# Performance work log

Measured on AMD Instinct MI355X. Metric: run time of the kernel, lower is better.

## Reference

```python
import jax, jax.numpy as jnp
import numpy as np

N, T, IN, E, H, OUT = 4096, 256, 2, 64, 128, 2


def setup_inputs() -> dict:
    key = jax.random.key(0)
    ks = jax.random.split(key, 10)
    s = 0.05
    return {
        "x": jax.random.normal(ks[0], (N, T, IN), dtype=jnp.float32),
        "W_in": jax.random.normal(ks[1], (E, IN), dtype=jnp.float32) * s,
        "b_in": jax.random.normal(ks[2], (E,), dtype=jnp.float32) * s,
        "W_ih": jax.random.normal(ks[3], (4 * H, E), dtype=jnp.float32) * s,
        "W_hh": jax.random.normal(ks[4], (4 * H, H), dtype=jnp.float32) * s,
        "b_ih": jax.random.normal(ks[5], (4 * H,), dtype=jnp.float32) * s,
        "b_hh": jax.random.normal(ks[6], (4 * H,), dtype=jnp.float32) * s,
        "W_out": jax.random.normal(ks[7], (OUT, H), dtype=jnp.float32) * s,
        "b_out": jax.random.normal(ks[8], (OUT,), dtype=jnp.float32) * s,
    }


def reference(x, W_in, b_in, W_ih, W_hh, b_ih, b_hh, W_out, b_out):
    # x: [N, T, IN]. burn_in_steps = -1 (teacher forcing every step), use_mask=False,
    # rel_out=True, rtype='lstm'. PyTorch LSTMCell gate order: i, f, g, o.
    n = x.shape[0]
    h0 = jnp.zeros((n, H), dtype=x.dtype)
    c0 = jnp.zeros((n, H), dtype=x.dtype)

    def step(carry, x_t):
        h, c = carry
        embed = jax.nn.relu(x_t @ W_in.T + b_in)              # [N, E]
        gates = embed @ W_ih.T + b_ih + h @ W_hh.T + b_hh     # [N, 4H]
        i, f, g, o = jnp.split(gates, 4, axis=-1)
        i = jax.nn.sigmoid(i)
        f = jax.nn.sigmoid(f)
        g = jnp.tanh(g)
        o = jax.nn.sigmoid(o)
        c_new = f * c + i * g
        h_new = o * jnp.tanh(c_new)
        y_t = h_new @ W_out.T + b_out + x_t                   # rel_out: residual add
        return (h_new, c_new), y_t

    xs = jnp.swapaxes(x, 0, 1)                                 # [T, N, IN]
    _, ys = jax.lax.scan(step, (h0, c0), xs)                   # ys: [T, N, OUT]
    return jnp.swapaxes(ys, 0, 1)                              # [N, T, OUT]
```

## Files before the change

### kernel.cpp

```cpp
#include <hip/hip_runtime.h>


#define T_LEN 256
#define ROWS  16
#define NT    4
#define KT    6
#define ASTR  200

typedef __attribute__((ext_vector_type(8))) short short8;
typedef __attribute__((ext_vector_type(4))) float f32x4;
typedef __attribute__((ext_vector_type(2))) float f32x2;

__device__ __forceinline__ unsigned short f2bf(float f) {
  unsigned u = __builtin_bit_cast(unsigned, f);
  u += 0x7fffu + ((u >> 16) & 1u);
  return (unsigned short)(u >> 16);
}
__device__ __forceinline__ f32x2 exp2v(f32x2 x) {
  return (f32x2){__builtin_amdgcn_exp2f(x[0]), __builtin_amdgcn_exp2f(x[1])};
}
__device__ __forceinline__ f32x2 rcpv(f32x2 x) {
  return (f32x2){__builtin_amdgcn_rcpf(x[0]), __builtin_amdgcn_rcpf(x[1])};
}

__device__ __forceinline__ f32x2 ewpair(f32x2 i, f32x2 f, f32x2 g, f32x2 o, f32x2& c) {
  const float K1 = -1.4426950408889634f, K2 = -2.8853900817779268f;
  f32x2 ei = exp2v(i * K1);
  f32x2 ef = exp2v(f * K1);
  f32x2 eg = exp2v(g * K2);
  f32x2 eo = exp2v(o * K1);
  f32x2 t1 = ei + 1.f, tf = ef + 1.f, t2 = eg + 1.f, t3 = 1.f - eg, to = eo + 1.f;
  f32x2 q1 = t1 * t2;
  f32x2 num = c * q1 + t3 * tf;
  f32x2 cn = num * rcpv(q1 * tf);
  c = cn;
  f32x2 cc = __builtin_elementwise_min(
      __builtin_elementwise_max(cn, (f32x2){-20.f, -20.f}), (f32x2){20.f, 20.f});
  f32x2 ec = exp2v(cc * K2);
  return (1.f - ec) * rcpv(to * (ec + 1.f));
}

__global__ __launch_bounds__(512, 2) void lstm_persist(
    const float* __restrict__ x,    const float* __restrict__ W_in,
    const float* __restrict__ b_in, const float* __restrict__ W_ih,
    const float* __restrict__ W_hh, const float* __restrict__ b_ih,
    const float* __restrict__ b_hh, const float* __restrict__ W_out,
    const float* __restrict__ b_out, float* __restrict__ out)
{
  __shared__ __align__(16) float xsT[2 * T_LEN][ROWS];
  __shared__ __align__(16) unsigned short Abuf[3][ROWS][ASTR];
  __shared__ float WinS[128];
  __shared__ float binS[64];

  const int tid  = threadIdx.x;
  const int w    = tid >> 6;
  const int l    = tid & 63;
  const int l15  = l & 15;
  const int lq   = l >> 4;
  const int u    = w * 16 + l15;
  const int row0 = lq * 4;

  const float* xg = x + (size_t)blockIdx.x * ROWS * 2 * T_LEN;
  for (int i = tid; i < ROWS * 2 * T_LEN / 4; i += 512) {
    float4 v = ((const float4*)xg)[i];
    int fi = i * 4, r = fi >> 9, c0 = fi & 511;
    xsT[c0][r] = v.x; xsT[c0 + 1][r] = v.y; xsT[c0 + 2][r] = v.z; xsT[c0 + 3][r] = v.w;
  }
  if (tid < 128) WinS[tid] = W_in[tid];
  if (tid < 64)  binS[tid] = b_in[tid];

  short8 fb[NT][KT];
  f32x4  biasv[NT];
  #pragma unroll
  for (int t = 0; t < NT; ++t) {
    const int grow = t * 128 + u;
    const float bv = b_ih[grow] + b_hh[grow];
    biasv[t] = (f32x4){bv, bv, bv, bv};
    #pragma unroll
    for (int kt = 0; kt < KT; ++kt) {
      const int kk = kt * 32 + lq * 8;
      const float* src = (kk < 64) ? (W_ih + grow * 64 + kk)
                                   : (W_hh + grow * 128 + (kk - 64));
      float4 lo = *(const float4*)src;
      float4 hi = *(const float4*)(src + 4);
      short8 f;
      f[0] = (short)f2bf(lo.x); f[1] = (short)f2bf(lo.y);
      f[2] = (short)f2bf(lo.z); f[3] = (short)f2bf(lo.w);
      f[4] = (short)f2bf(hi.x); f[5] = (short)f2bf(hi.y);
      f[6] = (short)f2bf(hi.z); f[7] = (short)f2bf(hi.w);
      fb[t][kt] = f;
    }
  }
  short8 fbY[4];
  #pragma unroll
  for (int kt = 0; kt < 4; ++kt) {
    short8 fy = {0, 0, 0, 0, 0, 0, 0, 0};
    if (l15 < 2) {
      const float* src = W_out + l15 * 128 + kt * 32 + lq * 8;
      #pragma unroll
      for (int j = 0; j < 8; ++j) fy[j] = (short)f2bf(src[j]);
    }
    fbY[kt] = fy;
  }
  const float bout_r = (l15 < 2) ? b_out[l15] : 0.f;

  __syncthreads();

  auto embed_to = [&](unsigned short (*buf)[ASTR], int t) {
    const int r = tid >> 5;
    const float x0 = xsT[2 * t][r], x1 = xsT[2 * t + 1][r];
    #pragma unroll
    for (int s = 0; s < 2; ++s) {
      const int e = (tid & 31) + s * 32;
      float v = fmaf(x1, WinS[2 * e + 1], fmaf(x0, WinS[2 * e], binS[e]));
      buf[r][e] = f2bf(v > 0.f ? v : 0.f);
    }
  };

  for (int i = tid; i < ROWS * 128; i += 512)
    Abuf[0][i >> 7][64 + (i & 127)] = 0;
  embed_to(Abuf[0], 0);
  embed_to(Abuf[1], 1);
  __syncthreads();

  f32x4 accA[NT], accB[NT];
  {
    const short8 a0 = *(const short8*)&Abuf[0][l15][lq * 8];
    const short8 a1 = *(const short8*)&Abuf[0][l15][32 + lq * 8];
    #pragma unroll
    for (int n = 0; n < NT; ++n) {
      f32x4 acc = biasv[n];
      acc = __builtin_amdgcn_mfma_f32_16x16x32_bf16(a0, fb[n][0], acc, 0, 0, 0);
      acc = __builtin_amdgcn_mfma_f32_16x16x32_bf16(a1, fb[n][1], acc, 0, 0, 0);
      accA[n] = acc;
    }
  }

  f32x2 c01 = {0.f, 0.f}, c23 = {0.f, 0.f};
  const size_t obase = (size_t)blockIdx.x * ROWS * 2 * T_LEN;

  auto step = [&](int t, unsigned short (*bR)[ASTR], unsigned short (*bW)[ASTR],
                  unsigned short (*bE)[ASTR], f32x4 (&accC)[NT], f32x4 (&accN)[NT]) {
    short8 ah[4];
    #pragma unroll
    for (int kt = 0; kt < 4; ++kt)
      ah[kt] = *(const short8*)&bR[l15][(kt + 2) * 32 + lq * 8];
    #pragma unroll
    for (int kt = 0; kt < 4; ++kt) {
      #pragma unroll
      for (int n = 0; n < NT; ++n)
        accC[n] = __builtin_amdgcn_mfma_f32_16x16x32_bf16(ah[kt], fb[n][kt + 2], accC[n], 0, 0, 0);
    }

    f32x4 accY;
    if (w == 0) {
      const int tt = (t > 0) ? t - 1 : 0;
      #pragma unroll
      for (int q = 0; q < 4; ++q)
        accY[q] = (l15 < 2) ? (bout_r + xsT[2 * tt + l15][row0 + q]) : 0.f;
      #pragma unroll
      for (int kt = 0; kt < 4; ++kt)
        accY = __builtin_amdgcn_mfma_f32_16x16x32_bf16(ah[kt], fbY[kt], accY, 0, 0, 0);
    }

    if (t + 1 < T_LEN) {
      const short8 a0 = *(const short8*)&bW[l15][lq * 8];
      const short8 a1 = *(const short8*)&bW[l15][32 + lq * 8];
      #pragma unroll
      for (int n = 0; n < NT; ++n) {
        f32x4 acc = biasv[n];
        acc = __builtin_amdgcn_mfma_f32_16x16x32_bf16(a0, fb[n][0], acc, 0, 0, 0);
        acc = __builtin_amdgcn_mfma_f32_16x16x32_bf16(a1, fb[n][1], acc, 0, 0, 0);
        accN[n] = acc;
      }
    }

    {
      f32x2 i01 = {accC[0][0], accC[0][1]}, f01 = {accC[1][0], accC[1][1]};
      f32x2 g01 = {accC[2][0], accC[2][1]}, o01 = {accC[3][0], accC[3][1]};
      f32x2 h01 = ewpair(i01, f01, g01, o01, c01);
      bW[row0 + 0][64 + u] = f2bf(h01[0]);
      bW[row0 + 1][64 + u] = f2bf(h01[1]);
      f32x2 i23 = {accC[0][2], accC[0][3]}, f23 = {accC[1][2], accC[1][3]};
      f32x2 g23 = {accC[2][2], accC[2][3]}, o23 = {accC[3][2], accC[3][3]};
      f32x2 h23 = ewpair(i23, f23, g23, o23, c23);
      bW[row0 + 2][64 + u] = f2bf(h23[0]);
      bW[row0 + 3][64 + u] = f2bf(h23[1]);
    }

    if (t + 2 < T_LEN) embed_to(bE, t + 2);

    if (w == 0 && t > 0 && l15 < 2) {
      #pragma unroll
      for (int q = 0; q < 4; ++q)
        out[obase + (size_t)(row0 + q) * (2 * T_LEN) + 2 * (t - 1) + l15] = accY[q];
    }

    __syncthreads();
  };

  unsigned short (*B0)[ASTR] = Abuf[0];
  unsigned short (*B1)[ASTR] = Abuf[1];
  unsigned short (*B2)[ASTR] = Abuf[2];

  for (int t = 0; t < 252; t += 6) {
    step(t + 0, B0, B1, B2, accA, accB);
    step(t + 1, B1, B2, B0, accB, accA);
    step(t + 2, B2, B0, B1, accA, accB);
    step(t + 3, B0, B1, B2, accB, accA);
    step(t + 4, B1, B2, B0, accA, accB);
    step(t + 5, B2, B0, B1, accB, accA);
  }
  step(252, B0, B1, B2, accA, accB);
  step(253, B1, B2, B0, accB, accA);
  step(254, B2, B0, B1, accA, accB);
  step(255, B0, B1, B2, accB, accA);

  if (w == 0) {
    short8 ah[4];
    #pragma unroll
    for (int kt = 0; kt < 4; ++kt)
      ah[kt] = *(const short8*)&Abuf[1][l15][(kt + 2) * 32 + lq * 8];
    f32x4 accY;
    #pragma unroll
    for (int q = 0; q < 4; ++q)
      accY[q] = (l15 < 2) ? (bout_r + xsT[2 * 255 + l15][row0 + q]) : 0.f;
    #pragma unroll
    for (int kt = 0; kt < 4; ++kt)
      accY = __builtin_amdgcn_mfma_f32_16x16x32_bf16(ah[kt], fbY[kt], accY, 0, 0, 0);
    if (l15 < 2) {
      #pragma unroll
      for (int q = 0; q < 4; ++q)
        out[obase + (size_t)(row0 + q) * (2 * T_LEN) + 2 * 255 + l15] = accY[q];
    }
  }
}

extern "C" void kernel_launch(void* const* d_in, const int* in_sizes, int n_in,
                              void* d_out, int out_size, void* d_ws, size_t ws_size,
                              hipStream_t stream) {
  const float* x     = (const float*)d_in[0];
  const float* W_in  = (const float*)d_in[1];
  const float* b_in  = (const float*)d_in[2];
  const float* W_ih  = (const float*)d_in[3];
  const float* W_hh  = (const float*)d_in[4];
  const float* b_ih  = (const float*)d_in[5];
  const float* b_hh  = (const float*)d_in[6];
  const float* W_out = (const float*)d_in[7];
  const float* b_out = (const float*)d_in[8];
  float* out = (float*)d_out;

  lstm_persist<<<dim3(256), dim3(512), 0, stream>>>(
      x, W_in, b_in, W_ih, W_hh, b_ih, b_hh, W_out, b_out, out);
}
```

Before: 262.8 us.

## Split LSTM gate K-reduction across two wave halves with LDS partial exchange

Doubles the block to 1024 threads and splits the per-step recurrent MFMA reduction along K between two 8-wave halves. Partial gate sums are exchanged through a new LDS buffer, and each half then runs the elementwise cell update for two of the four rows. The A buffer also switches to an XOR-swizzled layout to cut bank conflicts. The aim is to halve the serial MFMA chain per wave on the critical recurrent path, at the cost of an extra __syncthreads per step and extra LDS traffic.

Result: slower. 494.2 us (+88.0%).

```diff
diff --git a/kernel.cpp b/kernel.cpp
--- a/kernel.cpp
+++ b/kernel.cpp
@@ -2,10 +2,7 @@
 
 
 #define T_LEN 256
-#define ROWS  16
-#define NT    4
-#define KT    6
-#define ASTR  200
+#define NROW  16
 
 typedef __attribute__((ext_vector_type(8))) short short8;
 typedef __attribute__((ext_vector_type(4))) float f32x4;
@@ -40,28 +37,31 @@
   return (1.f - ec) * rcpv(to * (ec + 1.f));
 }
 
-__global__ __launch_bounds__(512, 2) void lstm_persist(
+__global__ __launch_bounds__(1024, 4) void lstm_persist(
     const float* __restrict__ x,    const float* __restrict__ W_in,
     const float* __restrict__ b_in, const float* __restrict__ W_ih,
     const float* __restrict__ W_hh, const float* __restrict__ b_ih,
     const float* __restrict__ b_hh, const float* __restrict__ W_out,
     const float* __restrict__ b_out, float* __restrict__ out)
 {
-  __shared__ __align__(16) float xsT[2 * T_LEN][ROWS];
-  __shared__ __align__(16) unsigned short Abuf[3][ROWS][ASTR];
+  __shared__ __align__(16) float xsT[2 * T_LEN][NROW];
+  __shared__ __align__(16) unsigned short Abuf[3][NROW * 192];
+  __shared__ __align__(16) float Xbuf[2][8][64 * 12];
+  __shared__ __align__(16) float Ybuf[64 * 4];
   __shared__ float WinS[128];
   __shared__ float binS[64];
 
-  const int tid  = threadIdx.x;
-  const int w    = tid >> 6;
-  const int l    = tid & 63;
-  const int l15  = l & 15;
-  const int lq   = l >> 4;
-  const int u    = w * 16 + l15;
-  const int row0 = lq * 4;
-
-  const float* xg = x + (size_t)blockIdx.x * ROWS * 2 * T_LEN;
-  for (int i = tid; i < ROWS * 2 * T_LEN / 4; i += 512) {
+  const int tid = threadIdx.x;
+  const int w   = tid >> 6;
+  const int l   = tid & 63;
+  const int l15 = l & 15;
+  const int lq  = l >> 4;
+  const int kh  = w >> 3;
+  const int w8  = w & 7;
+  const int u   = w8 * 16 + l15;
+
+  const float* xg = x + (size_t)blockIdx.x * NROW * 2 * T_LEN;
+  for (int i = tid; i < NROW * 2 * T_LEN / 4; i += 1024) {
     float4 v = ((const float4*)xg)[i];
     int fi = i * 4, r = fi >> 9, c0 = fi & 511;
     xsT[c0][r] = v.x; xsT[c0 + 1][r] = v.y; xsT[c0 + 2][r] = v.z; xsT[c0 + 3][r] = v.w;
@@ -69,16 +69,20 @@
   if (tid < 128) WinS[tid] = W_in[tid];
   if (tid < 64)  binS[tid] = b_in[tid];
 
-  short8 fb[NT][KT];
-  f32x4  biasv[NT];
+  const int kt0 = kh ? 1 : 0;
+  const int ktA = kh ? 4 : 2;
+  const int ktB = kh ? 5 : 3;
+
+  short8 fb[4][3];
+  float  bias4[4];
   #pragma unroll
-  for (int t = 0; t < NT; ++t) {
-    const int grow = t * 128 + u;
-    const float bv = b_ih[grow] + b_hh[grow];
-    biasv[t] = (f32x4){bv, bv, bv, bv};
-    #pragma unroll
-    for (int kt = 0; kt < KT; ++kt) {
-      const int kk = kt * 32 + lq * 8;
+  for (int g = 0; g < 4; ++g) {
+    const int grow = g * 128 + u;
+    bias4[g] = (kh == 0) ? (b_ih[grow] + b_hh[grow]) : 0.f;
+    const int kts[3] = {kt0, ktA, ktB};
+    #pragma unroll
+    for (int j = 0; j < 3; ++j) {
+      const int kk = kts[j] * 32 + lq * 8;
       const float* src = (kk < 64) ? (W_ih + grow * 64 + kk)
                                    : (W_hh + grow * 128 + (kk - 64));
       float4 lo = *(const float4*)src;
@@ -88,151 +92,165 @@
       f[2] = (short)f2bf(lo.z); f[3] = (short)f2bf(lo.w);
       f[4] = (short)f2bf(hi.x); f[5] = (short)f2bf(hi.y);
       f[6] = (short)f2bf(hi.z); f[7] = (short)f2bf(hi.w);
-      fb[t][kt] = f;
-    }
-  }
-  short8 fbY[4];
+      fb[g][j] = f;
+    }
+  }
+  short8 fbY[2];
   #pragma unroll
-  for (int kt = 0; kt < 4; ++kt) {
+  for (int j = 0; j < 2; ++j) {
     short8 fy = {0, 0, 0, 0, 0, 0, 0, 0};
+    const int kt = ktA + j;
     if (l15 < 2) {
-      const float* src = W_out + l15 * 128 + kt * 32 + lq * 8;
+      const float* src = W_out + l15 * 128 + (kt - 2) * 32 + lq * 8;
       #pragma unroll
-      for (int j = 0; j < 8; ++j) fy[j] = (short)f2bf(src[j]);
-    }
-    fbY[kt] = fy;
+      for (int e = 0; e < 8; ++e) fy[e] = (short)f2bf(src[e]);
+    }
+    fbY[j] = fy;
   }
   const float bout_r = (l15 < 2) ? b_out[l15] : 0.f;
 
   __syncthreads();
 
-  auto embed_to = [&](unsigned short (*buf)[ASTR], int t) {
-    const int r = tid >> 5;
-    const float x0 = xsT[2 * t][r], x1 = xsT[2 * t + 1][r];
-    #pragma unroll
-    for (int s = 0; s < 2; ++s) {
-      const int e = (tid & 31) + s * 32;
-      float v = fmaf(x1, WinS[2 * e + 1], fmaf(x0, WinS[2 * e], binS[e]));
-      buf[r][e] = f2bf(v > 0.f ? v : 0.f);
-    }
-  };
-
-  for (int i = tid; i < ROWS * 128; i += 512)
-    Abuf[0][i >> 7][64 + (i & 127)] = 0;
-  embed_to(Abuf[0], 0);
-  embed_to(Abuf[1], 1);
+  auto frag_read = [&](const unsigned short* buf, int kt) -> short8 {
+    return *(const short8*)&buf[l15 * 192 + (((kt * 4 + lq) ^ (l15 & 7)) * 8)];
+  };
+  auto embed1 = [&](unsigned short* buf, int t) {
+    const float x0 = xsT[2 * t][w], x1 = xsT[2 * t + 1][w];
+    float v = fmaf(x1, WinS[2 * l + 1], fmaf(x0, WinS[2 * l], binS[l]));
+    v = v > 0.f ? v : 0.f;
+    buf[w * 192 + (((l >> 3) ^ (w & 7)) * 8) + (l & 7)] = f2bf(v);
+  };
+  auto hwrite = [&](unsigned short* buf, int r, float v) {
+    buf[r * 192 + (((8 + (u >> 3)) ^ (r & 7)) * 8) + (u & 7)] = f2bf(v);
+  };
+
+  ((unsigned*)&Abuf[0][(tid >> 6) * 192 + 64])[tid & 63] = 0u;
+  embed1(Abuf[0], 0);
+  embed1(Abuf[1], 1);
   __syncthreads();
 
-  f32x4 accA[NT], accB[NT];
+  f32x4 accA[4], accB[4];
   {
-    const short8 a0 = *(const short8*)&Abuf[0][l15][lq * 8];
-    const short8 a1 = *(const short8*)&Abuf[0][l15][32 + lq * 8];
-    #pragma unroll
-    for (int n = 0; n < NT; ++n) {
-      f32x4 acc = biasv[n];
-      acc = __builtin_amdgcn_mfma_f32_16x16x32_bf16(a0, fb[n][0], acc, 0, 0, 0);
-      acc = __builtin_amdgcn_mfma_f32_16x16x32_bf16(a1, fb[n][1], acc, 0, 0, 0);
-      accA[n] = acc;
-    }
-  }
-
-  f32x2 c01 = {0.f, 0.f}, c23 = {0.f, 0.f};
-  const size_t obase = (size_t)blockIdx.x * ROWS * 2 * T_LEN;
-
-  auto step = [&](int t, unsigned short (*bR)[ASTR], unsigned short (*bW)[ASTR],
-                  unsigned short (*bE)[ASTR], f32x4 (&accC)[NT], f32x4 (&accN)[NT]) {
-    short8 ah[4];
-    #pragma unroll
-    for (int kt = 0; kt < 4; ++kt)
-      ah[kt] = *(const short8*)&bR[l15][(kt + 2) * 32 + lq * 8];
-    #pragma unroll
-    for (int kt = 0; kt < 4; ++kt) {
+    const short8 a0 = frag_read(Abuf[0], kt0);
+    #pragma unroll
+    for (int g = 0; g < 4; ++g) {
+      f32x4 s = (f32x4){bias4[g], bias4[g], bias4[g], bias4[g]};
+      accA[g] = __builtin_amdgcn_mfma_f32_16x16x32_bf16(a0, fb[g][0], s, 0, 0, 0);
+    }
+  }
+
+  f32x2 c01 = {0.f, 0.f};
+  const size_t obase = (size_t)blockIdx.x * NROW * 2 * T_LEN;
+  const int qa = kh ? 0 : 2;
+  const int qk = kh ? 2 : 0;
+  const int r0 = lq * 4 + 2 * kh;
+
+  auto step = [&](int t, unsigned short* bR, unsigned short* bW, unsigned short* bE,
+                  f32x4 (&accC)[4], f32x4 (&accN)[4]) {
+    const short8 ahA = frag_read(bR, ktA);
+    const short8 ahB = frag_read(bR, ktB);
+    #pragma unroll
+    for (int g = 0; g < 4; ++g)
+      accC[g] = __builtin_amdgcn_mfma_f32_16x16x32_bf16(ahA, fb[g][1], accC[g], 0, 0, 0);
+    #pragma unroll
+    for (int g = 0; g < 4; ++g)
+      accC[g] = __builtin_amdgcn_mfma_f32_16x16x32_bf16(ahB, fb[g][2], accC[g], 0, 0, 0);
+
+    f32x4 accY;
+    if (w8 == 0) {
+      if (kh == 0) {
+        const int tt = (t > 0) ? t - 1 : 0;
+        #pragma unroll
+        for (int q = 0; q < 4; ++q)
+          accY[q] = (l15 < 2) ? (bout_r + xsT[2 * tt + l15][lq * 4 + q]) : 0.f;
+      } else {
+        accY = (f32x4){0.f, 0.f, 0.f, 0.f};
+      }
+      accY = __builtin_amdgcn_mfma_f32_16x16x32_bf16(ahA, fbY[0], accY, 0, 0, 0);
+      accY = __builtin_amdgcn_mfma_f32_16x16x32_bf16(ahB, fbY[1], accY, 0, 0, 0);
+      if (kh == 1) *(f32x4*)&Ybuf[l * 4] = accY;
+    }
+
+    {
+      float* xb = &Xbuf[kh][w8][l * 12];
+      *(f32x4*)xb       = (f32x4){accC[0][qa], accC[0][qa + 1], accC[1][qa], accC[1][qa + 1]};
+      *(f32x4*)(xb + 4) = (f32x4){accC[2][qa], accC[2][qa + 1], accC[3][qa], accC[3][qa + 1]};
+    }
+
+    if (t + 1 < T_LEN) {
+      const short8 a0 = frag_read(bW, kt0);
       #pragma unroll
-      for (int n = 0; n < NT; ++n)
-        accC[n] = __builtin_amdgcn_mfma_f32_16x16x32_bf16(ah[kt], fb[n][kt + 2], accC[n], 0, 0, 0);
-    }
-
-    f32x4 accY;
-    if (w == 0) {
-      const int tt = (t > 0) ? t - 1 : 0;
+      for (int g = 0; g < 4; ++g) {
+        f32x4 s = (f32x4){bias4[g], bias4[g], bias4[g], bias4[g]};
+        accN[g] = __builtin_amdgcn_mfma_f32_16x16x32_bf16(a0, fb[g][0], s, 0, 0, 0);
+      }
+    }
+
+    __syncthreads();
+
+    {
+      const float* xb = &Xbuf[kh ^ 1][w8][l * 12];
+      const f32x4 p0 = *(const f32x4*)xb;
+      const f32x4 p1 = *(const f32x4*)(xb + 4);
+      f32x2 iv = {accC[0][qk] + p0[0], accC[0][qk + 1] + p0[1]};
+      f32x2 fv = {accC[1][qk] + p0[2], accC[1][qk + 1] + p0[3]};
+      f32x2 gv = {accC[2][qk] + p1[0], accC[2][qk + 1] + p1[1]};
+      f32x2 ov = {accC[3][qk] + p1[2], accC[3][qk + 1] + p1[3]};
+      f32x2 hv = ewpair(iv, fv, gv, ov, c01);
+      hwrite(bW, r0,     hv[0]);
+      hwrite(bW, r0 + 1, hv[1]);
+    }
+
+    if (t + 2 < T_LEN) embed1(bE, t + 2);
+
+    if (w8 == 0 && kh == 0 && t > 0) {
+      const f32x4 py = *(const f32x4*)&Ybuf[l * 4];
+      if (l15 < 2) {
+        #pragma unroll
+        for (int q = 0; q < 4; ++q)
+          out[obase + (size_t)(lq * 4 + q) * (2 * T_LEN) + 2 * (t - 1) + l15] = accY[q] + py[q];
+      }
+    }
+
+    __syncthreads();
+  };
+
+  unsigned short* A0 = Abuf[0];
+  unsigned short* A1 = Abuf[1];
+  unsigned short* A2 = Abuf[2];
+
+  for (int t = 0; t < 252; t += 6) {
+    step(t + 0, A0, A1, A2, accA, accB);
+    step(t + 1, A1, A2, A0, accB, accA);
+    step(t + 2, A2, A0, A1, accA, accB);
+    step(t + 3, A0, A1, A2, accB, accA);
+    step(t + 4, A1, A2, A0, accA, accB);
+    step(t + 5, A2, A0, A1, accB, accA);
+  }
+  step(252, A0, A1, A2, accA, accB);
+  step(253, A1, A2, A0, accB, accA);
+  step(254, A2, A0, A1, accA, accB);
+  step(255, A0, A1, A2, accB, accA);
+
+  f32x4 accYe = (f32x4){0.f, 0.f, 0.f, 0.f};
+  if (w8 == 0) {
+    const short8 ahA = frag_read(A1, ktA);
+    const short8 ahB = frag_read(A1, ktB);
+    if (kh == 0) {
       #pragma unroll
       for (int q = 0; q < 4; ++q)
-        accY[q] = (l15 < 2) ? (bout_r + xsT[2 * tt + l15][row0 + q]) : 0.f;
-      #pragma unroll
-      for (int kt = 0; kt < 4; ++kt)
-        accY = __builtin_amdgcn_mfma_f32_16x16x32_bf16(ah[kt], fbY[kt], accY, 0, 0, 0);
-    }
-
-    if (t + 1 < T_LEN) {
-      const short8 a0 = *(const short8*)&bW[l15][lq * 8];
-      const short8 a1 = *(const short8*)&bW[l15][32 + lq * 8];
-      #pragma unroll
-      for (int n = 0; n < NT; ++n) {
-        f32x4 acc = biasv[n];
-        acc = __builtin_amdgcn_mfma_f32_16x16x32_bf16(a0, fb[n][0], acc, 0, 0, 0);
-        acc = __builtin_amdgcn_mfma_f32_16x16x32_bf16(a1, fb[n][1], acc, 0, 0, 0);
-        accN[n] = acc;
-      }
-    }
-
-    {
-      f32x2 i01 = {accC[0][0], accC[0][1]}, f01 = {accC[1][0], accC[1][1]};
-      f32x2 g01 = {accC[2][0], accC[2][1]}, o01 = {accC[3][0], accC[3][1]};
-      f32x2 h01 = ewpair(i01, f01, g01, o01, c01);
-      bW[row0 + 0][64 + u] = f2bf(h01[0]);
-      bW[row0 + 1][64 + u] = f2bf(h01[1]);
-      f32x2 i23 = {accC[0][2], accC[0][3]}, f23 = {accC[1][2], accC[1][3]};
-      f32x2 g23 = {accC[2][2], accC[2][3]}, o23 = {accC[3][2], accC[3][3]};
-      f32x2 h23 = ewpair(i23, f23, g23, o23, c23);
-      bW[row0 + 2][64 + u] = f2bf(h23[0]);
-      bW[row0 + 3][64 + u] = f2bf(h23[1]);
-    }
-
-    if (t + 2 < T_LEN) embed_to(bE, t + 2);
-
-    if (w == 0 && t > 0 && l15 < 2) {
-      #pragma unroll
-      for (int q = 0; q < 4; ++q)
-        out[obase + (size_t)(row0 + q) * (2 * T_LEN) + 2 * (t - 1) + l15] = accY[q];
-    }
-
-    __syncthreads();
-  };
-
-  unsigned short (*B0)[ASTR] = Abuf[0];
-  unsigned short (*B1)[ASTR] = Abuf[1];
-  unsigned short (*B2)[ASTR] = Abuf[2];
-
-  for (int t = 0; t < 252; t += 6) {
-    step(t + 0, B0, B1, B2, accA, accB);
-    step(t + 1, B1, B2, B0, accB, accA);
-    step(t + 2, B2, B0, B1, accA, accB);
-    step(t + 3, B0, B1, B2, accB, accA);
-    step(t + 4, B1, B2, B0, accA, accB);
-    step(t + 5, B2, B0, B1, accB, accA);
-  }
-  step(252, B0, B1, B2, accA, accB);
-  step(253, B1, B2, B0, accB, accA);
-  step(254, B2, B0, B1, accA, accB);
-  step(255, B0, B1, B2, accB, accA);
-
-  if (w == 0) {
-    short8 ah[4];
-    #pragma unroll
-    for (int kt = 0; kt < 4; ++kt)
-      ah[kt] = *(const short8*)&Abuf[1][l15][(kt + 2) * 32 + lq * 8];
-    f32x4 accY;
+        accYe[q] = (l15 < 2) ? (bout_r + xsT[2 * 255 + l15][lq * 4 + q]) : 0.f;
+    }
+    accYe = __builtin_amdgcn_mfma_f32_16x16x32_bf16(ahA, fbY[0], accYe, 0, 0, 0);
+    accYe = __builtin_amdgcn_mfma_f32_16x16x32_bf16(ahB, fbY[1], accYe, 0, 0, 0);
+    if (kh == 1) *(f32x4*)&Ybuf[l * 4] = accYe;
+  }
+  __syncthreads();
+  if (w8 == 0 && kh == 0 && l15 < 2) {
+    const f32x4 py = *(const f32x4*)&Ybuf[l * 4];
     #pragma unroll
     for (int q = 0; q < 4; ++q)
-      accY[q] = (l15 < 2) ? (bout_r + xsT[2 * 255 + l15][row0 + q]) : 0.f;
-    #pragma unroll
-    for (int kt = 0; kt < 4; ++kt)
-      accY = __builtin_amdgcn_mfma_f32_16x16x32_bf16(ah[kt], fbY[kt], accY, 0, 0, 0);
-    if (l15 < 2) {
-      #pragma unroll
-      for (int q = 0; q < 4; ++q)
-        out[obase + (size_t)(row0 + q) * (2 * T_LEN) + 2 * 255 + l15] = accY[q];
-    }
+      out[obase + (size_t)(lq * 4 + q) * (2 * T_LEN) + 2 * 255 + l15] = accYe[q] + py[q];
   }
 }
 
@@ -250,6 +268,6 @@
   const float* b_out = (const float*)d_in[8];
   float* out = (float*)d_out;
 
-  lstm_persist<<<dim3(256), dim3(512), 0, stream>>>(
+  lstm_persist<<<dim3(256), dim3(1024), 0, stream>>>(
       x, W_in, b_in, W_ih, W_hh, b_ih, b_hh, W_out, b_out, out);
 }
```

## Split warps into recurrent-unit and input-projection producer roles with swizzled LDS

Applied to the files above, without the earlier changes.

The block grows to 1024 threads. Eight waves run only the recurrent W_hh matmul and the gate elementwise work. The other eight waves precompute the input-embedding projection (W_ih times embed plus bias) one step ahead into a double-buffered fp32 LDS buffer, and also compute the embedding two steps ahead. This takes the W_ih MFMAs and the embedding ALU work off the critical recurrent path, and the smaller per-wave weight set frees registers. In exchange it adds LDS traffic for the gx handoff and more waves per barrier. It also XOR-swizzles the h/embed LDS layouts to avoid bank conflicts and moves the W_out fragments into LDS.

Result: slower. 518.6 us (+97.4%).

```diff
diff --git a/kernel.cpp b/kernel.cpp
--- a/kernel.cpp
+++ b/kernel.cpp
@@ -2,10 +2,6 @@
 
 
 #define T_LEN 256
-#define ROWS  16
-#define NT    4
-#define KT    6
-#define ASTR  200
 
 typedef __attribute__((ext_vector_type(8))) short short8;
 typedef __attribute__((ext_vector_type(4))) float f32x4;
@@ -40,28 +36,45 @@
   return (1.f - ec) * rcpv(to * (ec + 1.f));
 }
 
-__global__ __launch_bounds__(512, 2) void lstm_persist(
+__device__ __forceinline__ short8 packbf8(const float* src) {
+  float4 lo = *(const float4*)src;
+  float4 hi = *(const float4*)(src + 4);
+  short8 f;
+  f[0] = (short)f2bf(lo.x); f[1] = (short)f2bf(lo.y);
+  f[2] = (short)f2bf(lo.z); f[3] = (short)f2bf(lo.w);
+  f[4] = (short)f2bf(hi.x); f[5] = (short)f2bf(hi.y);
+  f[6] = (short)f2bf(hi.z); f[7] = (short)f2bf(hi.w);
+  return f;
+}
+
+#define MFMA __builtin_amdgcn_mfma_f32_16x16x32_bf16
+
+__global__ __launch_bounds__(1024, 4) void lstm_persist(
     const float* __restrict__ x,    const float* __restrict__ W_in,
     const float* __restrict__ b_in, const float* __restrict__ W_ih,
     const float* __restrict__ W_hh, const float* __restrict__ b_ih,
     const float* __restrict__ b_hh, const float* __restrict__ W_out,
     const float* __restrict__ b_out, float* __restrict__ out)
 {
-  __shared__ __align__(16) float xsT[2 * T_LEN][ROWS];
-  __shared__ __align__(16) unsigned short Abuf[3][ROWS][ASTR];
+  __shared__ __align__(16) float xsT[2 * T_LEN][16];
   __shared__ float WinS[128];
   __shared__ float binS[64];
-
-  const int tid  = threadIdx.x;
-  const int w    = tid >> 6;
-  const int l    = tid & 63;
-  const int l15  = l & 15;
-  const int lq   = l >> 4;
-  const int u    = w * 16 + l15;
-  const int row0 = lq * 4;
-
-  const float* xg = x + (size_t)blockIdx.x * ROWS * 2 * T_LEN;
-  for (int i = tid; i < ROWS * 2 * T_LEN / 4; i += 512) {
+  __shared__ __align__(16) unsigned short embB[2][16 * 64];
+  __shared__ __align__(16) unsigned short hB[2][16 * 128];
+  __shared__ __align__(16) float gx[2][512 * 20];
+  __shared__ __align__(16) unsigned short fyB[4 * 64 * 8];
+
+  const int tid = threadIdx.x;
+  const int w   = tid >> 6;
+  const int l   = tid & 63;
+  const int l15 = l & 15;
+  const int lq  = l >> 4;
+  const int w8  = w & 7;
+  const bool is_unit = (w < 8);
+
+  const float* xg = x + (size_t)blockIdx.x * (16 * 2 * T_LEN);
+  #pragma unroll
+  for (int i = tid; i < 2048; i += 1024) {
     float4 v = ((const float4*)xg)[i];
     int fi = i * 4, r = fi >> 9, c0 = fi & 511;
     xsT[c0][r] = v.x; xsT[c0 + 1][r] = v.y; xsT[c0 + 2][r] = v.z; xsT[c0 + 3][r] = v.w;
@@ -69,169 +82,192 @@
   if (tid < 128) WinS[tid] = W_in[tid];
   if (tid < 64)  binS[tid] = b_in[tid];
 
-  short8 fb[NT][KT];
-  f32x4  biasv[NT];
+  short8 FB[16];
+  float  biasC[4];
+  float  bout_r = 0.f;
+  if (is_unit) {
+    #pragma unroll
+    for (int g = 0; g < 4; ++g) {
+      const int grow = g * 128 + 16 * w8 + l15;
+      #pragma unroll
+      for (int kt = 0; kt < 4; ++kt)
+        FB[g * 4 + kt] = packbf8(W_hh + grow * 128 + kt * 32 + lq * 8);
+    }
+    bout_r = (l15 < 2) ? b_out[l15] : 0.f;
+    if (w == 0) {
+      #pragma unroll
+      for (int kt = 0; kt < 4; ++kt) {
+        short8 fy = {0, 0, 0, 0, 0, 0, 0, 0};
+        if (l15 < 2) fy = packbf8(W_out + l15 * 128 + kt * 32 + lq * 8);
+        *(short8*)&fyB[(kt * 64 + l) * 8] = fy;
+      }
+    }
+  } else {
+    #pragma unroll
+    for (int tt = 0; tt < 4; ++tt) {
+      const int col = 64 * w8 + 16 * tt + l15;
+      biasC[tt] = b_ih[col] + b_hh[col];
+      #pragma unroll
+      for (int kt = 0; kt < 2; ++kt)
+        FB[tt * 2 + kt] = packbf8(W_ih + col * 64 + kt * 32 + lq * 8);
+    }
+  }
+  __syncthreads();
+
+  {
+    const int tt = tid >> 9;
+    const int s  = tid & 511;
+    const int r = s >> 5, e0 = (s & 31) * 2;
+    const float x0 = xsT[2 * tt][r], x1 = xsT[2 * tt + 1][r];
+    float v0 = fmaf(x1, WinS[2 * e0 + 1], fmaf(x0, WinS[2 * e0], binS[e0]));
+    float v1 = fmaf(x1, WinS[2 * e0 + 3], fmaf(x0, WinS[2 * e0 + 2], binS[e0 + 1]));
+    v0 = v0 > 0.f ? v0 : 0.f; v1 = v1 > 0.f ? v1 : 0.f;
+    const int ei = r * 64 + (((e0 >> 3) ^ (r & 7)) * 8) + (e0 & 7);
+    *(unsigned*)&embB[tt][ei] = (unsigned)f2bf(v0) | ((unsigned)f2bf(v1) << 16);
+    ((unsigned*)&hB[0][0])[tid] = 0u;
+  }
+  __syncthreads();
+
+  if (!is_unit) {
+    const short8 ae0 = *(const short8*)&embB[0][l15 * 64 + ((lq ^ (l15 & 7)) * 8)];
+    const short8 ae1 = *(const short8*)&embB[0][l15 * 64 + (((4 + lq) ^ (l15 & 7)) * 8)];
+    #pragma unroll
+    for (int tt = 0; tt < 4; ++tt) {
+      f32x4 a = (f32x4){biasC[tt], biasC[tt], biasC[tt], biasC[tt]};
+      a = MFMA(ae0, FB[tt * 2 + 0], a, 0, 0, 0);
+      a = MFMA(ae1, FB[tt * 2 + 1], a, 0, 0, 0);
+      *(f32x4*)&gx[0][(64 * w8 + 16 * tt + l15) * 20 + lq * 4] = a;
+    }
+  }
+  __syncthreads();
+
+  f32x2 c01 = {0.f, 0.f}, c23 = {0.f, 0.f};
+  const size_t obase = (size_t)blockIdx.x * (16 * 2 * T_LEN);
+  const int u = 16 * w8 + l15;
+  int hw[4];
   #pragma unroll
-  for (int t = 0; t < NT; ++t) {
-    const int grow = t * 128 + u;
-    const float bv = b_ih[grow] + b_hh[grow];
-    biasv[t] = (f32x4){bv, bv, bv, bv};
-    #pragma unroll
-    for (int kt = 0; kt < KT; ++kt) {
-      const int kk = kt * 32 + lq * 8;
-      const float* src = (kk < 64) ? (W_ih + grow * 64 + kk)
-                                   : (W_hh + grow * 128 + (kk - 64));
-      float4 lo = *(const float4*)src;
-      float4 hi = *(const float4*)(src + 4);
-      short8 f;
-      f[0] = (short)f2bf(lo.x); f[1] = (short)f2bf(lo.y);
-      f[2] = (short)f2bf(lo.z); f[3] = (short)f2bf(lo.w);
-      f[4] = (short)f2bf(hi.x); f[5] = (short)f2bf(hi.y);
-      f[6] = (short)f2bf(hi.z); f[7] = (short)f2bf(hi.w);
-      fb[t][kt] = f;
-    }
-  }
-  short8 fbY[4];
-  #pragma unroll
-  for (int kt = 0; kt < 4; ++kt) {
-    short8 fy = {0, 0, 0, 0, 0, 0, 0, 0};
+  for (int q = 0; q < 4; ++q) {
+    const int r = lq * 4 + q;
+    hw[q] = r * 128 + (((u >> 3) ^ (r & 7)) * 8) + (u & 7);
+  }
+
+  for (int t = 0; t < T_LEN; ++t) {
+    const int p = t & 1;
+    if (is_unit) {
+      const float* gxp = &gx[p][(16 * w8 + l15) * 20 + lq * 4];
+      f32x4 acc0 = *(const f32x4*)(gxp + 0 * 2560);
+      f32x4 acc1 = *(const f32x4*)(gxp + 1 * 2560);
+      f32x4 acc2 = *(const f32x4*)(gxp + 2 * 2560);
+      f32x4 acc3 = *(const f32x4*)(gxp + 3 * 2560);
+      const unsigned short* hb = hB[p];
+      const short8 ah0 = *(const short8*)&hb[l15 * 128 + (((0 * 4 + lq) ^ (l15 & 7)) * 8)];
+      const short8 ah1 = *(const short8*)&hb[l15 * 128 + (((1 * 4 + lq) ^ (l15 & 7)) * 8)];
+      const short8 ah2 = *(const short8*)&hb[l15 * 128 + (((2 * 4 + lq) ^ (l15 & 7)) * 8)];
+      const short8 ah3 = *(const short8*)&hb[l15 * 128 + (((3 * 4 + lq) ^ (l15 & 7)) * 8)];
+      acc0 = MFMA(ah0, FB[0],  acc0, 0, 0, 0);
+      acc1 = MFMA(ah0, FB[4],  acc1, 0, 0, 0);
+      acc2 = MFMA(ah0, FB[8],  acc2, 0, 0, 0);
+      acc3 = MFMA(ah0, FB[12], acc3, 0, 0, 0);
+      acc0 = MFMA(ah1, FB[1],  acc0, 0, 0, 0);
+      acc1 = MFMA(ah1, FB[5],  acc1, 0, 0, 0);
+      acc2 = MFMA(ah1, FB[9],  acc2, 0, 0, 0);
+      acc3 = MFMA(ah1, FB[13], acc3, 0, 0, 0);
+      acc0 = MFMA(ah2, FB[2],  acc0, 0, 0, 0);
+      acc1 = MFMA(ah2, FB[6],  acc1, 0, 0, 0);
+      acc2 = MFMA(ah2, FB[10], acc2, 0, 0, 0);
+      acc3 = MFMA(ah2, FB[14], acc3, 0, 0, 0);
+      acc0 = MFMA(ah3, FB[3],  acc0, 0, 0, 0);
+      acc1 = MFMA(ah3, FB[7],  acc1, 0, 0, 0);
+      acc2 = MFMA(ah3, FB[11], acc2, 0, 0, 0);
+      acc3 = MFMA(ah3, FB[15], acc3, 0, 0, 0);
+
+      if (w == 0) {
+        const int ttm = t ? t - 1 : 0;
+        f32x4 accY;
+        #pragma unroll
+        for (int q = 0; q < 4; ++q)
+          accY[q] = (l15 < 2) ? (bout_r + xsT[2 * ttm + l15][lq * 4 + q]) : 0.f;
+        const short8 fy0 = *(const short8*)&fyB[(0 * 64 + l) * 8];
+        const short8 fy1 = *(const short8*)&fyB[(1 * 64 + l) * 8];
+        const short8 fy2 = *(const short8*)&fyB[(2 * 64 + l) * 8];
+        const short8 fy3 = *(const short8*)&fyB[(3 * 64 + l) * 8];
+        accY = MFMA(ah0, fy0, accY, 0, 0, 0);
+        accY = MFMA(ah1, fy1, accY, 0, 0, 0);
+        accY = MFMA(ah2, fy2, accY, 0, 0, 0);
+        accY = MFMA(ah3, fy3, accY, 0, 0, 0);
+        if (t > 0 && l15 < 2) {
+          #pragma unroll
+          for (int q = 0; q < 4; ++q)
+            out[obase + (size_t)(lq * 4 + q) * (2 * T_LEN) + 2 * (t - 1) + l15] = accY[q];
+        }
+      }
+
+      unsigned short* hbW = hB[p ^ 1];
+      {
+        f32x2 iv = {acc0[0], acc0[1]}, fv = {acc1[0], acc1[1]};
+        f32x2 gv = {acc2[0], acc2[1]}, ov = {acc3[0], acc3[1]};
+        f32x2 h01 = ewpair(iv, fv, gv, ov, c01);
+        hbW[hw[0]] = f2bf(h01[0]);
+        hbW[hw[1]] = f2bf(h01[1]);
+      }
+      {
+        f32x2 iv = {acc0[2], acc0[3]}, fv = {acc1[2], acc1[3]};
+        f32x2 gv = {acc2[2], acc2[3]}, ov = {acc3[2], acc3[3]};
+        f32x2 h23 = ewpair(iv, fv, gv, ov, c23);
+        hbW[hw[2]] = f2bf(h23[0]);
+        hbW[hw[3]] = f2bf(h23[1]);
+      }
+    } else {
+      if (t < T_LEN - 1) {
+        const int pn = (t + 1) & 1;
+        const unsigned short* eb = embB[pn];
+        const short8 ae0 = *(const short8*)&eb[l15 * 64 + ((lq ^ (l15 & 7)) * 8)];
+        const short8 ae1 = *(const short8*)&eb[l15 * 64 + (((4 + lq) ^ (l15 & 7)) * 8)];
+        #pragma unroll
+        for (int tt = 0; tt < 4; ++tt) {
+          f32x4 a = (f32x4){biasC[tt], biasC[tt], biasC[tt], biasC[tt]};
+          a = MFMA(ae0, FB[tt * 2 + 0], a, 0, 0, 0);
+          a = MFMA(ae1, FB[tt * 2 + 1], a, 0, 0, 0);
+          *(f32x4*)&gx[pn][(64 * w8 + 16 * tt + l15) * 20 + lq * 4] = a;
+        }
+      }
+      if (t < T_LEN - 2) {
+        const int s = w8 * 64 + l;
+        const int r = s >> 5, e0 = (s & 31) * 2;
+        const int te = t + 2;
+        const float x0 = xsT[2 * te][r], x1 = xsT[2 * te + 1][r];
+        float v0 = fmaf(x1, WinS[2 * e0 + 1], fmaf(x0, WinS[2 * e0], binS[e0]));
+        float v1 = fmaf(x1, WinS[2 * e0 + 3], fmaf(x0, WinS[2 * e0 + 2], binS[e0 + 1]));
+        v0 = v0 > 0.f ? v0 : 0.f; v1 = v1 > 0.f ? v1 : 0.f;
+        const int ei = r * 64 + (((e0 >> 3) ^ (r & 7)) * 8) + (e0 & 7);
+        *(unsigned*)&embB[t & 1][ei] = (unsigned)f2bf(v0) | ((unsigned)f2bf(v1) << 16);
+      }
+    }
+    __syncthreads();
+  }
+
+  if (w == 0) {
+    const unsigned short* hb = hB[0];
+    const short8 ah0 = *(const short8*)&hb[l15 * 128 + (((0 * 4 + lq) ^ (l15 & 7)) * 8)];
+    const short8 ah1 = *(const short8*)&hb[l15 * 128 + (((1 * 4 + lq) ^ (l15 & 7)) * 8)];
+    const short8 ah2 = *(const short8*)&hb[l15 * 128 + (((2 * 4 + lq) ^ (l15 & 7)) * 8)];
+    const short8 ah3 = *(const short8*)&hb[l15 * 128 + (((3 * 4 + lq) ^ (l15 & 7)) * 8)];
+    f32x4 accY;
+    #pragma unroll
+    for (int q = 0; q < 4; ++q)
+      accY[q] = (l15 < 2) ? (bout_r + xsT[2 * 255 + l15][lq * 4 + q]) : 0.f;
+    const short8 fy0 = *(const short8*)&fyB[(0 * 64 + l) * 8];
+    const short8 fy1 = *(const short8*)&fyB[(1 * 64 + l) * 8];
+    const short8 fy2 = *(const short8*)&fyB[(2 * 64 + l) * 8];
+    const short8 fy3 = *(const short8*)&fyB[(3 * 64 + l) * 8];
+    accY = MFMA(ah0, fy0, accY, 0, 0, 0);
+    accY = MFMA(ah1, fy1, accY, 0, 0, 0);
+    accY = MFMA(ah2, fy2, accY, 0, 0, 0);
+    accY = MFMA(ah3, fy3, accY, 0, 0, 0);
     if (l15 < 2) {
-      const float* src = W_out + l15 * 128 + kt * 32 + lq * 8;
-      #pragma unroll
-      for (int j = 0; j < 8; ++j) fy[j] = (short)f2bf(src[j]);
-    }
-    fbY[kt] = fy;
-  }
-  const float bout_r = (l15 < 2) ? b_out[l15] : 0.f;
-
-  __syncthreads();
-
-  auto embed_to = [&](unsigned short (*buf)[ASTR], int t) {
-    const int r = tid >> 5;
-    const float x0 = xsT[2 * t][r], x1 = xsT[2 * t + 1][r];
-    #pragma unroll
-    for (int s = 0; s < 2; ++s) {
-      const int e = (tid & 31) + s * 32;
-      float v = fmaf(x1, WinS[2 * e + 1], fmaf(x0, WinS[2 * e], binS[e]));
-      buf[r][e] = f2bf(v > 0.f ? v : 0.f);
-    }
-  };
-
-  for (int i = tid; i < ROWS * 128; i += 512)
-    Abuf[0][i >> 7][64 + (i & 127)] = 0;
-  embed_to(Abuf[0], 0);
-  embed_to(Abuf[1], 1);
-  __syncthreads();
-
-  f32x4 accA[NT], accB[NT];
-  {
-    const short8 a0 = *(const short8*)&Abuf[0][l15][lq * 8];
-    const short8 a1 = *(const short8*)&Abuf[0][l15][32 + lq * 8];
-    #pragma unroll
-    for (int n = 0; n < NT; ++n) {
-      f32x4 acc = biasv[n];
-      acc = __builtin_amdgcn_mfma_f32_16x16x32_bf16(a0, fb[n][0], acc, 0, 0, 0);
-      acc = __builtin_amdgcn_mfma_f32_16x16x32_bf16(a1, fb[n][1], acc, 0, 0, 0);
-      accA[n] = acc;
-    }
-  }
-
-  f32x2 c01 = {0.f, 0.f}, c23 = {0.f, 0.f};
-  const size_t obase = (size_t)blockIdx.x * ROWS * 2 * T_LEN;
-
-  auto step = [&](int t, unsigned short (*bR)[ASTR], unsigned short (*bW)[ASTR],
-                  unsigned short (*bE)[ASTR], f32x4 (&accC)[NT], f32x4 (&accN)[NT]) {
-    short8 ah[4];
-    #pragma unroll
-    for (int kt = 0; kt < 4; ++kt)
-      ah[kt] = *(const short8*)&bR[l15][(kt + 2) * 32 + lq * 8];
-    #pragma unroll
-    for (int kt = 0; kt < 4; ++kt) {
-      #pragma unroll
-      for (int n = 0; n < NT; ++n)
-        accC[n] = __builtin_amdgcn_mfma_f32_16x16x32_bf16(ah[kt], fb[n][kt + 2], accC[n], 0, 0, 0);
-    }
-
-    f32x4 accY;
-    if (w == 0) {
-      const int tt = (t > 0) ? t - 1 : 0;
       #pragma unroll
       for (int q = 0; q < 4; ++q)
-        accY[q] = (l15 < 2) ? (bout_r + xsT[2 * tt + l15][row0 + q]) : 0.f;
-      #pragma unroll
-      for (int kt = 0; kt < 4; ++kt)
-        accY = __builtin_amdgcn_mfma_f32_16x16x32_bf16(ah[kt], fbY[kt], accY, 0, 0, 0);
-    }
-
-    if (t + 1 < T_LEN) {
-      const short8 a0 = *(const short8*)&bW[l15][lq * 8];
-      const short8 a1 = *(const short8*)&bW[l15][32 + lq * 8];
-      #pragma unroll
-      for (int n = 0; n < NT; ++n) {
-        f32x4 acc = biasv[n];
-        acc = __builtin_amdgcn_mfma_f32_16x16x32_bf16(a0, fb[n][0], acc, 0, 0, 0);
-        acc = __builtin_amdgcn_mfma_f32_16x16x32_bf16(a1, fb[n][1], acc, 0, 0, 0);
-        accN[n] = acc;
-      }
-    }
-
-    {
-      f32x2 i01 = {accC[0][0], accC[0][1]}, f01 = {accC[1][0], accC[1][1]};
-      f32x2 g01 = {accC[2][0], accC[2][1]}, o01 = {accC[3][0], accC[3][1]};
-      f32x2 h01 = ewpair(i01, f01, g01, o01, c01);
-      bW[row0 + 0][64 + u] = f2bf(h01[0]);
-      bW[row0 + 1][64 + u] = f2bf(h01[1]);
-      f32x2 i23 = {accC[0][2], accC[0][3]}, f23 = {accC[1][2], accC[1][3]};
-      f32x2 g23 = {accC[2][2], accC[2][3]}, o23 = {accC[3][2], accC[3][3]};
-      f32x2 h23 = ewpair(i23, f23, g23, o23, c23);
-      bW[row0 + 2][64 + u] = f2bf(h23[0]);
-      bW[row0 + 3][64 + u] = f2bf(h23[1]);
-    }
-
-    if (t + 2 < T_LEN) embed_to(bE, t + 2);
-
-    if (w == 0 && t > 0 && l15 < 2) {
-      #pragma unroll
-      for (int q = 0; q < 4; ++q)
-        out[obase + (size_t)(row0 + q) * (2 * T_LEN) + 2 * (t - 1) + l15] = accY[q];
-    }
-
-    __syncthreads();
-  };
-
-  unsigned short (*B0)[ASTR] = Abuf[0];
-  unsigned short (*B1)[ASTR] = Abuf[1];
-  unsigned short (*B2)[ASTR] = Abuf[2];
-
-  for (int t = 0; t < 252; t += 6) {
-    step(t + 0, B0, B1, B2, accA, accB);
-    step(t + 1, B1, B2, B0, accB, accA);
-    step(t + 2, B2, B0, B1, accA, accB);
-    step(t + 3, B0, B1, B2, accB, accA);
-    step(t + 4, B1, B2, B0, accA, accB);
-    step(t + 5, B2, B0, B1, accB, accA);
-  }
-  step(252, B0, B1, B2, accA, accB);
-  step(253, B1, B2, B0, accB, accA);
-  step(254, B2, B0, B1, accA, accB);
-  step(255, B0, B1, B2, accB, accA);
-
-  if (w == 0) {
-    short8 ah[4];
-    #pragma unroll
-    for (int kt = 0; kt < 4; ++kt)
-      ah[kt] = *(const short8*)&Abuf[1][l15][(kt + 2) * 32 + lq * 8];
-    f32x4 accY;
-    #pragma unroll
-    for (int q = 0; q < 4; ++q)
-      accY[q] = (l15 < 2) ? (bout_r + xsT[2 * 255 + l15][row0 + q]) : 0.f;
-    #pragma unroll
-    for (int kt = 0; kt < 4; ++kt)
-      accY = __builtin_amdgcn_mfma_f32_16x16x32_bf16(ah[kt], fbY[kt], accY, 0, 0, 0);
-    if (l15 < 2) {
-      #pragma unroll
-      for (int q = 0; q < 4; ++q)
-        out[obase + (size_t)(row0 + q) * (2 * T_LEN) + 2 * 255 + l15] = accY[q];
+        out[obase + (size_t)(lq * 4 + q) * (2 * T_LEN) + 2 * 255 + l15] = accY[q];
     }
   }
 }
@@ -250,6 +286,6 @@
   const float* b_out = (const float*)d_in[8];
   float* out = (float*)d_out;
 
-  lstm_persist<<<dim3(256), dim3(512), 0, stream>>>(
+  lstm_persist<<<dim3(256), dim3(1024), 0, stream>>>(
       x, W_in, b_in, W_ih, W_hh, b_ih, b_hh, W_out, b_out, out);
 }
```

## Split recurrent MFMA chain into two accumulators and rotate output-projection wave

Applied to the files above, without the earlier changes.

The recurrent h·W_hh product is split into two independent accumulator chains (k-tiles 0-1 and 2-3) that are summed before the gate nonlinearity. This shortens the dependent MFMA chain on the critical path of each timestep. The output projection, previously always done by wave 0, now rotates across the 8 waves by timestep to spread its extra MFMA and store work. The embedding and h writes use packed v_cvt_pk_bf16_f32 conversions, and the launch attributes are expressed as amdgpu waves_per_eu, at the cost of more accumulator registers.

Result: no change. 267.1 us (+1.6%).

```diff
diff --git a/kernel.cpp b/kernel.cpp
--- a/kernel.cpp
+++ b/kernel.cpp
@@ -3,8 +3,6 @@
 
 #define T_LEN 256
 #define ROWS  16
-#define NT    4
-#define KT    6
 #define ASTR  200
 
 typedef __attribute__((ext_vector_type(8))) short short8;
@@ -40,7 +38,22 @@
   return (1.f - ec) * rcpv(to * (ec + 1.f));
 }
 
-__global__ __launch_bounds__(512, 2) void lstm_persist(
+__device__ __forceinline__ short8 packbf8(const float* src) {
+  float4 lo = *(const float4*)src;
+  float4 hi = *(const float4*)(src + 4);
+  short8 f;
+  f[0] = (short)f2bf(lo.x); f[1] = (short)f2bf(lo.y);
+  f[2] = (short)f2bf(lo.z); f[3] = (short)f2bf(lo.w);
+  f[4] = (short)f2bf(hi.x); f[5] = (short)f2bf(hi.y);
+  f[6] = (short)f2bf(hi.z); f[7] = (short)f2bf(hi.w);
+  return f;
+}
+
+#define MFMA __builtin_amdgcn_mfma_f32_16x16x32_bf16
+
+__global__ void __attribute__((amdgpu_flat_work_group_size(512, 512),
+                               amdgpu_waves_per_eu(2, 2)))
+lstm_persist(
     const float* __restrict__ x,    const float* __restrict__ W_in,
     const float* __restrict__ b_in, const float* __restrict__ W_ih,
     const float* __restrict__ W_hh, const float* __restrict__ b_ih,
@@ -61,6 +74,7 @@
   const int row0 = lq * 4;
 
   const float* xg = x + (size_t)blockIdx.x * ROWS * 2 * T_LEN;
+  #pragma unroll
   for (int i = tid; i < ROWS * 2 * T_LEN / 4; i += 512) {
     float4 v = ((const float4*)xg)[i];
     int fi = i * 4, r = fi >> 9, c0 = fi & 511;
@@ -69,37 +83,25 @@
   if (tid < 128) WinS[tid] = W_in[tid];
   if (tid < 64)  binS[tid] = b_in[tid];
 
-  short8 fb[NT][KT];
-  f32x4  biasv[NT];
+  short8 fb[4][6];
+  float  bias[4];
   #pragma unroll
-  for (int t = 0; t < NT; ++t) {
-    const int grow = t * 128 + u;
-    const float bv = b_ih[grow] + b_hh[grow];
-    biasv[t] = (f32x4){bv, bv, bv, bv};
-    #pragma unroll
-    for (int kt = 0; kt < KT; ++kt) {
+  for (int g = 0; g < 4; ++g) {
+    const int grow = g * 128 + u;
+    bias[g] = b_ih[grow] + b_hh[grow];
+    #pragma unroll
+    for (int kt = 0; kt < 6; ++kt) {
       const int kk = kt * 32 + lq * 8;
       const float* src = (kk < 64) ? (W_ih + grow * 64 + kk)
                                    : (W_hh + grow * 128 + (kk - 64));
-      float4 lo = *(const float4*)src;
-      float4 hi = *(const float4*)(src + 4);
-      short8 f;
-      f[0] = (short)f2bf(lo.x); f[1] = (short)f2bf(lo.y);
-      f[2] = (short)f2bf(lo.z); f[3] = (short)f2bf(lo.w);
-      f[4] = (short)f2bf(hi.x); f[5] = (short)f2bf(hi.y);
-      f[6] = (short)f2bf(hi.z); f[7] = (short)f2bf(hi.w);
-      fb[t][kt] = f;
+      fb[g][kt] = packbf8(src);
     }
   }
   short8 fbY[4];
   #pragma unroll
   for (int kt = 0; kt < 4; ++kt) {
     short8 fy = {0, 0, 0, 0, 0, 0, 0, 0};
-    if (l15 < 2) {
-      const float* src = W_out + l15 * 128 + kt * 32 + lq * 8;
-      #pragma unroll
-      for (int j = 0; j < 8; ++j) fy[j] = (short)f2bf(src[j]);
-    }
+    if (l15 < 2) fy = packbf8(W_out + l15 * 128 + kt * 32 + lq * 8);
     fbY[kt] = fy;
   }
   const float bout_r = (l15 < 2) ? b_out[l15] : 0.f;
@@ -107,14 +109,16 @@
   __syncthreads();
 
   auto embed_to = [&](unsigned short (*buf)[ASTR], int t) {
-    const int r = tid >> 5;
+    const int r  = tid >> 5;
+    const int e0 = (tid & 31) * 2;
     const float x0 = xsT[2 * t][r], x1 = xsT[2 * t + 1][r];
-    #pragma unroll
-    for (int s = 0; s < 2; ++s) {
-      const int e = (tid & 31) + s * 32;
-      float v = fmaf(x1, WinS[2 * e + 1], fmaf(x0, WinS[2 * e], binS[e]));
-      buf[r][e] = f2bf(v > 0.f ? v : 0.f);
-    }
+    float v0 = fmaf(x1, WinS[2 * e0 + 1], fmaf(x0, WinS[2 * e0], binS[e0]));
+    float v1 = fmaf(x1, WinS[2 * e0 + 3], fmaf(x0, WinS[2 * e0 + 2], binS[e0 + 1]));
+    v0 = v0 > 0.f ? v0 : 0.f;
+    v1 = v1 > 0.f ? v1 : 0.f;
+    unsigned ep;
+    asm("v_cvt_pk_bf16_f32 %0, %1, %2" : "=v"(ep) : "v"(v0), "v"(v1));
+    *(unsigned*)&buf[r][e0] = ep;
   };
 
   for (int i = tid; i < ROWS * 128; i += 512)
@@ -123,16 +127,16 @@
   embed_to(Abuf[1], 1);
   __syncthreads();
 
-  f32x4 accA[NT], accB[NT];
+  f32x4 accA[4], accB[4];
   {
     const short8 a0 = *(const short8*)&Abuf[0][l15][lq * 8];
     const short8 a1 = *(const short8*)&Abuf[0][l15][32 + lq * 8];
     #pragma unroll
-    for (int n = 0; n < NT; ++n) {
-      f32x4 acc = biasv[n];
-      acc = __builtin_amdgcn_mfma_f32_16x16x32_bf16(a0, fb[n][0], acc, 0, 0, 0);
-      acc = __builtin_amdgcn_mfma_f32_16x16x32_bf16(a1, fb[n][1], acc, 0, 0, 0);
-      accA[n] = acc;
+    for (int g = 0; g < 4; ++g) {
+      f32x4 acc = (f32x4){bias[g], bias[g], bias[g], bias[g]};
+      acc = MFMA(a0, fb[g][0], acc, 0, 0, 0);
+      acc = MFMA(a1, fb[g][1], acc, 0, 0, 0);
+      accA[g] = acc;
     }
   }
 
@@ -140,60 +144,76 @@
   const size_t obase = (size_t)blockIdx.x * ROWS * 2 * T_LEN;
 
   auto step = [&](int t, unsigned short (*bR)[ASTR], unsigned short (*bW)[ASTR],
-                  unsigned short (*bE)[ASTR], f32x4 (&accC)[NT], f32x4 (&accN)[NT]) {
+                  unsigned short (*bE)[ASTR], f32x4 (&accC)[4], f32x4 (&accN)[4]) {
     short8 ah[4];
     #pragma unroll
     for (int kt = 0; kt < 4; ++kt)
       ah[kt] = *(const short8*)&bR[l15][(kt + 2) * 32 + lq * 8];
-    #pragma unroll
-    for (int kt = 0; kt < 4; ++kt) {
-      #pragma unroll
-      for (int n = 0; n < NT; ++n)
-        accC[n] = __builtin_amdgcn_mfma_f32_16x16x32_bf16(ah[kt], fb[n][kt + 2], accC[n], 0, 0, 0);
-    }
-
+
+    f32x4 accQ[4];
+    #pragma unroll
+    for (int g = 0; g < 4; ++g) {
+      accC[g] = MFMA(ah[0], fb[g][2], accC[g], 0, 0, 0);
+      accQ[g] = MFMA(ah[2], fb[g][4], (f32x4){0.f, 0.f, 0.f, 0.f}, 0, 0, 0);
+    }
+    #pragma unroll
+    for (int g = 0; g < 4; ++g) {
+      accC[g] = MFMA(ah[1], fb[g][3], accC[g], 0, 0, 0);
+      accQ[g] = MFMA(ah[3], fb[g][5], accQ[g], 0, 0, 0);
+    }
+
+    const int yw = t & 7;
     f32x4 accY;
-    if (w == 0) {
-      const int tt = (t > 0) ? t - 1 : 0;
+    if (w == yw) {
+      const int tt = t ? t - 1 : 0;
       #pragma unroll
       for (int q = 0; q < 4; ++q)
-        accY[q] = (l15 < 2) ? (bout_r + xsT[2 * tt + l15][row0 + q]) : 0.f;
-      #pragma unroll
-      for (int kt = 0; kt < 4; ++kt)
-        accY = __builtin_amdgcn_mfma_f32_16x16x32_bf16(ah[kt], fbY[kt], accY, 0, 0, 0);
+        accY[q] = (l15 < 2) ? (bout_r + xsT[2 * tt + l15][lq * 4 + q]) : 0.f;
+      accY = MFMA(ah[0], fbY[0], accY, 0, 0, 0);
+      accY = MFMA(ah[1], fbY[1], accY, 0, 0, 0);
+      accY = MFMA(ah[2], fbY[2], accY, 0, 0, 0);
+      accY = MFMA(ah[3], fbY[3], accY, 0, 0, 0);
     }
 
     if (t + 1 < T_LEN) {
       const short8 a0 = *(const short8*)&bW[l15][lq * 8];
       const short8 a1 = *(const short8*)&bW[l15][32 + lq * 8];
       #pragma unroll
-      for (int n = 0; n < NT; ++n) {
-        f32x4 acc = biasv[n];
-        acc = __builtin_amdgcn_mfma_f32_16x16x32_bf16(a0, fb[n][0], acc, 0, 0, 0);
-        acc = __builtin_amdgcn_mfma_f32_16x16x32_bf16(a1, fb[n][1], acc, 0, 0, 0);
-        accN[n] = acc;
+      for (int g = 0; g < 4; ++g) {
+        f32x4 acc = (f32x4){bias[g], bias[g], bias[g], bias[g]};
+        acc = MFMA(a0, fb[g][0], acc, 0, 0, 0);
+        acc = MFMA(a1, fb[g][1], acc, 0, 0, 0);
+        accN[g] = acc;
       }
     }
+
+    #pragma unroll
+    for (int g = 0; g < 4; ++g)
+      accC[g] += accQ[g];
 
     {
       f32x2 i01 = {accC[0][0], accC[0][1]}, f01 = {accC[1][0], accC[1][1]};
       f32x2 g01 = {accC[2][0], accC[2][1]}, o01 = {accC[3][0], accC[3][1]};
       f32x2 h01 = ewpair(i01, f01, g01, o01, c01);
-      bW[row0 + 0][64 + u] = f2bf(h01[0]);
-      bW[row0 + 1][64 + u] = f2bf(h01[1]);
+      unsigned hp;
+      asm("v_cvt_pk_bf16_f32 %0, %1, %2" : "=v"(hp) : "v"(h01[0]), "v"(h01[1]));
+      bW[row0 + 0][64 + u] = (unsigned short)hp;
+      bW[row0 + 1][64 + u] = (unsigned short)(hp >> 16);
       f32x2 i23 = {accC[0][2], accC[0][3]}, f23 = {accC[1][2], accC[1][3]};
       f32x2 g23 = {accC[2][2], accC[2][3]}, o23 = {accC[3][2], accC[3][3]};
       f32x2 h23 = ewpair(i23, f23, g23, o23, c23);
-      bW[row0 + 2][64 + u] = f2bf(h23[0]);
-      bW[row0 + 3][64 + u] = f2bf(h23[1]);
+      unsigned hq;
+      asm("v_cvt_pk_bf16_f32 %0, %1, %2" : "=v"(hq) : "v"(h23[0]), "v"(h23[1]));
+      bW[row0 + 2][64 + u] = (unsigned short)hq;
+      bW[row0 + 3][64 + u] = (unsigned short)(hq >> 16);
     }
 
     if (t + 2 < T_LEN) embed_to(bE, t + 2);
 
-    if (w == 0 && t > 0 && l15 < 2) {
+    if (w == yw && t > 0 && l15 < 2) {
       #pragma unroll
       for (int q = 0; q < 4; ++q)
-        out[obase + (size_t)(row0 + q) * (2 * T_LEN) + 2 * (t - 1) + l15] = accY[q];
+        out[obase + (size_t)(lq * 4 + q) * (2 * T_LEN) + 2 * (t - 1) + l15] = accY[q];
     }
 
     __syncthreads();
@@ -224,14 +244,15 @@
     f32x4 accY;
     #pragma unroll
     for (int q = 0; q < 4; ++q)
-      accY[q] = (l15 < 2) ? (bout_r + xsT[2 * 255 + l15][row0 + q]) : 0.f;
-    #pragma unroll
-    for (int kt = 0; kt < 4; ++kt)
-      accY = __builtin_amdgcn_mfma_f32_16x16x32_bf16(ah[kt], fbY[kt], accY, 0, 0, 0);
+      accY[q] = (l15 < 2) ? (bout_r + xsT[2 * 255 + l15][lq * 4 + q]) : 0.f;
+    accY = MFMA(ah[0], fbY[0], accY, 0, 0, 0);
+    accY = MFMA(ah[1], fbY[1], accY, 0, 0, 0);
+    accY = MFMA(ah[2], fbY[2], accY, 0, 0, 0);
+    accY = MFMA(ah[3], fbY[3], accY, 0, 0, 0);
     if (l15 < 2) {
       #pragma unroll
       for (int q = 0; q < 4; ++q)
-        out[obase + (size_t)(row0 + q) * (2 * T_LEN) + 2 * 255 + l15] = accY[q];
+        out[obase + (size_t)(lq * 4 + q) * (2 * T_LEN) + 2 * 255 + l15] = accY[q];
     }
   }
 }
```
